# Kernel tuning notes

Measured on AMD Instinct MI355X. Metric: run time of the kernel, lower is better.

Reference implementation:

```python
import jax, jax.numpy as jnp
import numpy as np
from jax import lax

N, E, F, H, B = 16384, 262144, 32, 128, 16
DI, DS, DC, DTR = 256, 16, 4, 8   # Mamba: d_inner=expand*H, d_state, d_conv, dt_rank=ceil(H/16)
NS, NC = 512, 8                   # num_stations, num line colors
EPS = 1e-5


def _forward(node_features, edge_index, batch, W_in, b_in, W_g1, b_g1, W_g2, b_g2,
             W_inproj, conv_w, conv_b, W_xproj, W_dt, b_dt, A_log, D_p, W_out,
             gamma, beta, Wc, bc, Wh, bh, Wt, bt, Wp1, bp1, Wp2, bp2, Wd, bd, Ws, bs):
    def gcn(x, W, b):
        # GCNConv with self-loops and symmetric normalization
        loops = jnp.arange(N)
        s = jnp.concatenate([edge_index[0], loops])
        d = jnp.concatenate([edge_index[1], loops])
        deg = jax.ops.segment_sum(jnp.ones(s.shape[0], x.dtype), d, num_segments=N)
        dinv = jnp.where(deg > 0, lax.rsqrt(deg), 0.0)
        xw = x @ W
        msg = xw[s] * (dinv[s] * dinv[d])[:, None]
        return jax.ops.segment_sum(msg, d, num_segments=N) + b

    h = jax.nn.relu(node_features @ W_in + b_in)
    h = jax.nn.relu(gcn(h, W_g1, b_g1))
    h_gnn = jax.nn.relu(gcn(h, W_g2, b_g2))

    # --- Mamba block over the node sequence (batch dim of 1, seq_len = N) ---
    xz = h_gnn @ W_inproj                      # (N, 2*DI)
    x, z = xz[:, :DI], xz[:, DI:]
    xp = jnp.pad(x, ((DC - 1, 0), (0, 0)))     # causal depthwise conv1d
    xc = conv_b + sum(xp[k:k + N] * conv_w[:, k] for k in range(DC))
    x = jax.nn.silu(xc)
    dbl = x @ W_xproj                          # (N, DTR + 2*DS)
    dt = jax.nn.softplus(dbl[:, :DTR] @ W_dt + b_dt)   # (N, DI)
    Bm = dbl[:, DTR:DTR + DS]                  # (N, DS)
    Cm = dbl[:, DTR + DS:]                     # (N, DS)
    A = -jnp.exp(A_log)                        # (DI, DS)
    dA = jnp.exp(dt[:, :, None] * A[None])     # (N, DI, DS)
    dBx = dt[:, :, None] * Bm[:, None, :] * x[:, :, None]

    def step(hst, t):
        dA_t, dBx_t, C_t = t
        hst = dA_t * hst + dBx_t               # (DI, DS)
        return hst, hst @ C_t                  # (DI,)

    _, ys = lax.scan(step, jnp.zeros((DI, DS), x.dtype), (dA, dBx, Cm))
    y = (ys + D_p * x) * jax.nn.silu(z)
    h_mamba = y @ W_out                        # (N, H)

    # residual + LayerNorm
    hh = h_gnn + h_mamba
    mu = hh.mean(-1, keepdims=True)
    var = ((hh - mu) ** 2).mean(-1, keepdims=True)
    h_final = (hh - mu) * lax.rsqrt(var + EPS) * gamma + beta

    # global_mean_pool per graph
    counts = jax.ops.segment_sum(jnp.ones(N, h_final.dtype), batch, num_segments=B)
    ge = jax.ops.segment_sum(h_final, batch, num_segments=B) / jnp.maximum(counts, 1.0)[:, None]

    # critic + all policy heads, concatenated: [1,4,3,NS,NS,NS,NC]
    return jnp.concatenate([ge @ Wc + bc, ge @ Wh + bh, ge @ Wt + bt,
                            ge @ Wp1 + bp1, ge @ Wp2 + bp2, ge @ Wd + bd,
                            ge @ Ws + bs], axis=-1)


def setup_inputs() -> dict:
    key = jax.random.key(0)
    ks = list(jax.random.split(key, 20))
    p = lambda i, shape, s=0.02: jax.random.normal(ks[i], shape, jnp.float32) * s
    return dict(
        node_features=jax.random.normal(ks[0], (N, F), jnp.float32),
        edge_index=jax.random.randint(ks[1], (2, E), 0, N),
        batch=jnp.sort(jax.random.randint(ks[2], (N,), 0, B)),
        W_in=p(3, (F, H)), b_in=jnp.zeros((H,), jnp.float32),
        W_g1=p(4, (H, H)), b_g1=jnp.zeros((H,), jnp.float32),
        W_g2=p(5, (H, H)), b_g2=jnp.zeros((H,), jnp.float32),
        W_inproj=p(6, (H, 2 * DI)),
        conv_w=p(7, (DI, DC)), conv_b=jnp.zeros((DI,), jnp.float32),
        W_xproj=p(8, (DI, DTR + 2 * DS)),
        W_dt=p(9, (DTR, DI)), b_dt=jnp.full((DI,), -4.0, jnp.float32),
        A_log=jnp.log(jnp.broadcast_to(jnp.arange(1.0, DS + 1.0, dtype=jnp.float32), (DI, DS))),
        D_p=jnp.ones((DI,), jnp.float32),
        W_out=p(10, (DI, H)),
        gamma=jnp.ones((H,), jnp.float32), beta=jnp.zeros((H,), jnp.float32),
        Wc=p(11, (H, 1)), bc=jnp.zeros((1,), jnp.float32),
        Wh=p(12, (H, 4)), bh=jnp.zeros((4,), jnp.float32),
        Wt=p(13, (H, 3)), bt=jnp.zeros((3,), jnp.float32),
        Wp1=p(14, (H, NS)), bp1=jnp.zeros((NS,), jnp.float32),
        Wp2=p(15, (H, NS)), bp2=jnp.zeros((NS,), jnp.float32),
        Wd=p(16, (H, NS)), bd=jnp.zeros((NS,), jnp.float32),
        Ws=p(17, (H, NC)), bs=jnp.zeros((NC,), jnp.float32),
    )


def reference(node_features, edge_index, batch, W_in, b_in, W_g1, b_g1, W_g2, b_g2,
              W_inproj, conv_w, conv_b, W_xproj, W_dt, b_dt, A_log, D_p, W_out,
              gamma, beta, Wc, bc, Wh, bh, Wt, bt, Wp1, bp1, Wp2, bp2, Wd, bd, Ws, bs):
    return _forward(node_features, edge_index, batch, W_in, b_in, W_g1, b_g1, W_g2, b_g2,
                    W_inproj, conv_w, conv_b, W_xproj, W_dt, b_dt, A_log, D_p, W_out,
                    gamma, beta, Wc, bc, Wh, bh, Wt, bt, Wp1, bp1, Wp2, bp2, Wd, bd, Ws, bs)
```

## Files before the change

kernel.cpp:

```cpp
#include <hip/hip_runtime.h>
#include <math.h>

#define NN 16384
#define EE 262144
#define FF 32
#define HH 128
#define BB 16
#define DI 256
#define DS 16
#define DC 4
#define DTR 8
#define OUTW 1552
#define NCH 512
#define CHLEN 32

__device__ __forceinline__ float siluf(float v) { return v / (1.f + __expf(-v)); }
__device__ __forceinline__ float softplusf(float v) {
    return fmaxf(v, 0.f) + __logf(1.f + __expf(-fabsf(v)));
}

__global__ void zero_kernel(int* __restrict__ cnt, float* __restrict__ ge,
                            int* __restrict__ counts) {
    int idx = blockIdx.x * blockDim.x + threadIdx.x;
    if (idx < NN) cnt[idx] = 0;
    if (idx < BB * HH) ge[idx] = 0.f;
    if (idx < BB) counts[idx] = 0;
}

__global__ void deg_kernel(const int* __restrict__ dst, int* __restrict__ cnt) {
    int e = blockIdx.x * blockDim.x + threadIdx.x;
    if (e < EE) atomicAdd(&cnt[dst[e]], 1);
}

__global__ __launch_bounds__(1024) void prefix_kernel(const int* __restrict__ cnt,
                                                      int* __restrict__ rowptr,
                                                      int* __restrict__ cursor,
                                                      float* __restrict__ dinv) {
    __shared__ int part[1024];
    int tid = threadIdx.x;
    int4 c4[4];
#pragma unroll
    for (int j = 0; j < 4; j++) c4[j] = ((const int4*)cnt)[tid * 4 + j];
    int v[16] = {c4[0].x, c4[0].y, c4[0].z, c4[0].w, c4[1].x, c4[1].y, c4[1].z, c4[1].w,
                 c4[2].x, c4[2].y, c4[2].z, c4[2].w, c4[3].x, c4[3].y, c4[3].z, c4[3].w};
    int s = 0;
#pragma unroll
    for (int j = 0; j < 16; j++) s += v[j];
    part[tid] = s;
    __syncthreads();
    for (int off = 1; off < 1024; off <<= 1) {
        int t = (tid >= off) ? part[tid - off] : 0;
        __syncthreads();
        part[tid] += t;
        __syncthreads();
    }
    int running = part[tid] - s;
    int rp[16];
    float dv[16];
#pragma unroll
    for (int j = 0; j < 16; j++) {
        rp[j] = running;
        running += v[j];
        dv[j] = rsqrtf((float)(v[j] + 1));
    }
#pragma unroll
    for (int j = 0; j < 4; j++) {
        int4 r4; r4.x = rp[j*4]; r4.y = rp[j*4+1]; r4.z = rp[j*4+2]; r4.w = rp[j*4+3];
        ((int4*)rowptr)[tid * 4 + j] = r4;
        ((int4*)cursor)[tid * 4 + j] = r4;
        float4 d4; d4.x = dv[j*4]; d4.y = dv[j*4+1]; d4.z = dv[j*4+2]; d4.w = dv[j*4+3];
        ((float4*)dinv)[tid * 4 + j] = d4;
    }
    if (tid == 1023) rowptr[NN] = part[1023];
}

__global__ void scatter_kernel(const int* __restrict__ src, const int* __restrict__ dst,
                               int* __restrict__ cursor, int* __restrict__ col) {
    int e = blockIdx.x * blockDim.x + threadIdx.x;
    if (e < EE) {
        int d = dst[e];
        int pos = atomicAdd(&cursor[d], 1);
        col[pos] = src[e];
    }
}

__global__ __launch_bounds__(256) void gemm_k(const float* __restrict__ A,
                                              const float* __restrict__ B,
                                              const float* __restrict__ bias,
                                              float* __restrict__ C,
                                              int M, int Nn, int K, int act) {
    __shared__ float As[16][68];
    __shared__ float Bs[16][68];
    int tid = threadIdx.x;
    int m0 = blockIdx.y * 64;
    int n0 = blockIdx.x * 64;
    int ty = tid >> 4, tx = tid & 15;
    float acc[4][4] = {{0.f}};
    for (int k0 = 0; k0 < K; k0 += 16) {
#pragma unroll
        for (int l = 0; l < 4; l++) {
            int idx = tid + l * 256;
            int i = idx >> 4, j = idx & 15;
            As[j][i] = A[(size_t)(m0 + i) * K + k0 + j];
        }
#pragma unroll
        for (int l = 0; l < 4; l++) {
            int idx = tid + l * 256;
            int i = idx >> 6, j = idx & 63;
            int n = n0 + j;
            Bs[i][j] = (n < Nn) ? B[(size_t)(k0 + i) * Nn + n] : 0.f;
        }
        __syncthreads();
#pragma unroll
        for (int kk = 0; kk < 16; kk++) {
            float4 a4 = *(const float4*)&As[kk][ty * 4];
            float4 b4 = *(const float4*)&Bs[kk][tx * 4];
            float av[4] = {a4.x, a4.y, a4.z, a4.w};
            float bv[4] = {b4.x, b4.y, b4.z, b4.w};
#pragma unroll
            for (int r = 0; r < 4; r++)
#pragma unroll
                for (int c = 0; c < 4; c++) acc[r][c] = fmaf(av[r], bv[c], acc[r][c]);
        }
        __syncthreads();
    }
    int nb = n0 + tx * 4;
    if (nb < Nn) {
        float4 bi4 = {0.f, 0.f, 0.f, 0.f};
        if (bias) bi4 = *(const float4*)&bias[nb];
#pragma unroll
        for (int r = 0; r < 4; r++) {
            int m = m0 + ty * 4 + r;
            float4 v;
            v.x = acc[r][0] + bi4.x; v.y = acc[r][1] + bi4.y;
            v.z = acc[r][2] + bi4.z; v.w = acc[r][3] + bi4.w;
            if (act == 1) {
                v.x = fmaxf(v.x, 0.f); v.y = fmaxf(v.y, 0.f);
                v.z = fmaxf(v.z, 0.f); v.w = fmaxf(v.w, 0.f);
            }
            *(float4*)&C[(size_t)m * Nn + nb] = v;
        }
    }
}

union SMemIn {
    struct { float Ns[64][33]; float Ws[32][132]; } s1;
    float Bs[16][68];
};

__global__ __launch_bounds__(256) void gemm_in_g1(const float* __restrict__ nf,
                                                  const float* __restrict__ W_in,
                                                  const float* __restrict__ b_in,
                                                  const float* __restrict__ W_g1,
                                                  float* __restrict__ out) {
    __shared__ SMemIn sm;
    __shared__ float Hs[128][68];
    int tid = threadIdx.x;
    int m0 = blockIdx.y * 64;
    int n0 = blockIdx.x * 64;
    int ty = tid >> 4, tx = tid & 15;
#pragma unroll
    for (int l = 0; l < 2; l++) {
        int q = tid + l * 256;
        int r = q >> 3, c4 = (q & 7) * 4;
        *(float4*)&sm.s1.Ns[r][c4] = *(const float4*)&nf[(size_t)(m0 + r) * FF + c4];
    }
#pragma unroll
    for (int l = 0; l < 4; l++) {
        int q = tid + l * 256;
        int r = q >> 5, c4 = (q & 31) * 4;
        *(float4*)&sm.s1.Ws[r][c4] = *(const float4*)&W_in[(size_t)r * HH + c4];
    }
    __syncthreads();
    {
        float4 b0 = *(const float4*)&b_in[tx * 4];
        float4 b1 = *(const float4*)&b_in[64 + tx * 4];
        float hacc[4][8];
#pragma unroll
        for (int r = 0; r < 4; r++) {
            hacc[r][0] = b0.x; hacc[r][1] = b0.y; hacc[r][2] = b0.z; hacc[r][3] = b0.w;
            hacc[r][4] = b1.x; hacc[r][5] = b1.y; hacc[r][6] = b1.z; hacc[r][7] = b1.w;
        }
#pragma unroll
        for (int k = 0; k < FF; k++) {
            float av[4];
#pragma unroll
            for (int r = 0; r < 4; r++) av[r] = sm.s1.Ns[ty * 4 + r][k];
            float wv[8];
#pragma unroll
            for (int c = 0; c < 4; c++) {
                wv[c]     = sm.s1.Ws[k][tx * 4 + c];
                wv[c + 4] = sm.s1.Ws[k][64 + tx * 4 + c];
            }
#pragma unroll
            for (int r = 0; r < 4; r++)
#pragma unroll
                for (int c = 0; c < 8; c++) hacc[r][c] = fmaf(av[r], wv[c], hacc[r][c]);
        }
#pragma unroll
        for (int r = 0; r < 4; r++)
#pragma unroll
            for (int c = 0; c < 4; c++) {
                Hs[tx * 4 + c][ty * 4 + r]      = fmaxf(hacc[r][c], 0.f);
                Hs[64 + tx * 4 + c][ty * 4 + r] = fmaxf(hacc[r][c + 4], 0.f);
            }
    }
    __syncthreads();
    float acc[4][4] = {{0.f}};
    for (int k0 = 0; k0 < HH; k0 += 16) {
        *(float4*)&sm.Bs[tid >> 4][(tid & 15) * 4] =
            *(const float4*)&W_g1[(size_t)(k0 + (tid >> 4)) * HH + n0 + (tid & 15) * 4];
        __syncthreads();
#pragma unroll
        for (int kk = 0; kk < 16; kk++) {
            float4 a4 = *(const float4*)&Hs[k0 + kk][ty * 4];
            float4 b4 = *(const float4*)&sm.Bs[kk][tx * 4];
            float av[4] = {a4.x, a4.y, a4.z, a4.w};
            float bv[4] = {b4.x, b4.y, b4.z, b4.w};
#pragma unroll
            for (int r = 0; r < 4; r++)
#pragma unroll
                for (int c = 0; c < 4; c++) acc[r][c] = fmaf(av[r], bv[c], acc[r][c]);
        }
        __syncthreads();
    }
#pragma unroll
    for (int r = 0; r < 4; r++) {
        int m = m0 + ty * 4 + r;
        float4 v;
        v.x = acc[r][0]; v.y = acc[r][1]; v.z = acc[r][2]; v.w = acc[r][3];
        *(float4*)&out[(size_t)m * HH + n0 + tx * 4] = v;
    }
}

__global__ __launch_bounds__(512, 4) void gemm_big512_t(const float* __restrict__ A,
                                                        const float* __restrict__ B,
                                                        float* __restrict__ CT,
                                                        int M, int Nn, int K) {
    __shared__ float As[16][132];
    __shared__ float Bs[16][132];
    int tid = threadIdx.x;
    int m0 = blockIdx.y * 128;
    int n0 = blockIdx.x * 128;
    int ty = tid >> 4;
    int tx = tid & 15;
    float acc[4][8] = {{0.f}};
    for (int k0 = 0; k0 < K; k0 += 16) {
        {
            int m = tid >> 2;
            int kc = (tid & 3) * 4;
            float4 a = *(const float4*)&A[(size_t)(m0 + m) * K + k0 + kc];
            As[kc + 0][m] = a.x; As[kc + 1][m] = a.y;
            As[kc + 2][m] = a.z; As[kc + 3][m] = a.w;
        }
        {
            int krow = tid >> 5;
            int c4 = (tid & 31) * 4;
            *(float4*)&Bs[krow][c4] = *(const float4*)&B[(size_t)(k0 + krow) * Nn + n0 + c4];
        }
        __syncthreads();
#pragma unroll
        for (int kk = 0; kk < 16; kk++) {
            float4 a4 = *(const float4*)&As[kk][ty * 4];
            float4 b0 = *(const float4*)&Bs[kk][tx * 4];
            float4 b1 = *(const float4*)&Bs[kk][64 + tx * 4];
            float av[4] = {a4.x, a4.y, a4.z, a4.w};
            float bv[8] = {b0.x, b0.y, b0.z, b0.w, b1.x, b1.y, b1.z, b1.w};
#pragma unroll
            for (int r = 0; r < 4; r++)
#pragma unroll
                for (int c = 0; c < 8; c++) acc[r][c] = fmaf(av[r], bv[c], acc[r][c]);
        }
        __syncthreads();
    }
#pragma unroll
    for (int cc = 0; cc < 4; cc++) {
        float4 v;
        v.x = acc[0][cc]; v.y = acc[1][cc]; v.z = acc[2][cc]; v.w = acc[3][cc];
        *(float4*)&CT[(size_t)(n0 + tx * 4 + cc) * NN + m0 + ty * 4] = v;
        float4 u;
        u.x = acc[0][cc + 4]; u.y = acc[1][cc + 4]; u.z = acc[2][cc + 4]; u.w = acc[3][cc + 4];
        *(float4*)&CT[(size_t)(n0 + 64 + tx * 4 + cc) * NN + m0 + ty * 4] = u;
    }
}

__global__ __launch_bounds__(256) void gemm_xz_dblt(const float* __restrict__ xzt,
                                                    const float* __restrict__ B,
                                                    const float* __restrict__ cw,
                                                    const float* __restrict__ cb,
                                                    float* __restrict__ xst,
                                                    float* __restrict__ dblt) {
    __shared__ float As[16][68];
    __shared__ float Bs[16][68];
    __shared__ float Raw[16][72];
    __shared__ float Ct[64][41];
    int tid = threadIdx.x;
    int m0 = blockIdx.x * 64;
    int ty = tid >> 4, tx = tid & 15;
    float acc[4][4] = {{0.f}};
    for (int k0 = 0; k0 < DI; k0 += 16) {
#pragma unroll
        for (int l = 0; l < 2; l++) {
            int idx = tid + l * 256;
            if (idx < 272) {
                int kk = idx / 17, j = idx % 17;
                int tcol = m0 - 4 + j * 4;
                float4 v;
                if (tcol >= 0) v = *(const float4*)&xzt[(size_t)(k0 + kk) * NN + tcol];
                else { v.x = 0.f; v.y = 0.f; v.z = 0.f; v.w = 0.f; }
                *(float4*)&Raw[kk][j * 4] = v;
            }
        }
#pragma unroll
        for (int l = 0; l < 4; l++) {
            int idx = tid + l * 256;
            int i2 = idx >> 6, j2 = idx & 63;
            Bs[i2][j2] = (j2 < 40) ? B[(size_t)(k0 + i2) * 40 + j2] : 0.f;
        }
        __syncthreads();
#pragma unroll
        for (int l = 0; l < 4; l++) {
            int kk = (tid >> 6) + l * 4;
            int i = tid & 63;
            int d = k0 + kk;
            float w0 = cw[d * DC + 0], w1 = cw[d * DC + 1];
            float w2 = cw[d * DC + 2], w3 = cw[d * DC + 3];
            float v = siluf(cb[d] + w0 * Raw[kk][i + 1] + w1 * Raw[kk][i + 2]
                                  + w2 * Raw[kk][i + 3] + w3 * Raw[kk][i + 4]);
            As[kk][i] = v;
            xst[(size_t)d * NN + m0 + i] = v;
        }
        __syncthreads();
#pragma unroll
        for (int kk = 0; kk < 16; kk++) {
            float4 a4 = *(const float4*)&As[kk][ty * 4];
            float4 b4 = *(const float4*)&Bs[kk][tx * 4];
            float av[4] = {a4.x, a4.y, a4.z, a4.w};
            float bv[4] = {b4.x, b4.y, b4.z, b4.w};
#pragma unroll
            for (int r = 0; r < 4; r++)
#pragma unroll
                for (int c = 0; c < 4; c++) acc[r][c] = fmaf(av[r], bv[c], acc[r][c]);
        }
        __syncthreads();
    }
    if (tx * 4 < 40) {
#pragma unroll
        for (int r = 0; r < 4; r++) {
            int m = ty * 4 + r;
            Ct[m][tx * 4 + 0] = acc[r][0];
            Ct[m][tx * 4 + 1] = acc[r][1];
            Ct[m][tx * 4 + 2] = acc[r][2];
            Ct[m][tx * 4 + 3] = acc[r][3];
        }
    }
    __syncthreads();
#pragma unroll
    for (int l = 0; l < 10; l++) {
        int idx = tid + l * 256;
        int n = idx >> 6, m = idx & 63;
        dblt[(size_t)n * NN + m0 + m] = Ct[m][n];
    }
}

__global__ __launch_bounds__(256) void gemm_at_ln_pool(const float* __restrict__ AT,
                                                       const float* __restrict__ B,
                                                       const float* __restrict__ hg,
                                                       const float* __restrict__ gamma,
                                                       const float* __restrict__ beta,
                                                       const int* __restrict__ batch,
                                                       float* __restrict__ ge,
                                                       int* __restrict__ counts) {
    __shared__ float As[16][36];
    __shared__ float Bs[16][132];
    __shared__ float lnb[32][132];
    __shared__ int gb[32];
    int tid = threadIdx.x;
    int m0 = blockIdx.x * 32;
    int ty = tid >> 4, tx = tid & 15;
    float acc[2][8] = {{0.f}};
    for (int k0 = 0; k0 < 256; k0 += 16) {
        {
            int idx = tid * 2;
            int kk = idx >> 5, i = idx & 31;
            As[kk][i] = AT[(size_t)(k0 + kk) * NN + m0 + i];
            As[kk][i + 1] = AT[(size_t)(k0 + kk) * NN + m0 + i + 1];
        }
        {
            int krow = tid >> 4;
            int c8 = (tid & 15) * 8;
            const float* bp = &B[(size_t)(k0 + krow) * HH + c8];
            *(float4*)&Bs[krow][c8] = *(const float4*)bp;
            *(float4*)&Bs[krow][c8 + 4] = *(const float4*)(bp + 4);
        }
        __syncthreads();
#pragma unroll
        for (int kk = 0; kk < 16; kk++) {
            float a0 = As[kk][ty * 2];
            float a1 = As[kk][ty * 2 + 1];
            float4 b0 = *(const float4*)&Bs[kk][tx * 4];
            float4 b1 = *(const float4*)&Bs[kk][64 + tx * 4];
            float bv[8] = {b0.x, b0.y, b0.z, b0.w, b1.x, b1.y, b1.z, b1.w};
#pragma unroll
            for (int c = 0; c < 8; c++) {
                acc[0][c] = fmaf(a0, bv[c], acc[0][c]);
                acc[1][c] = fmaf(a1, bv[c], acc[1][c]);
            }
        }
        __syncthreads();
    }
    if (tid < 32) gb[tid] = batch[m0 + tid];
    float4 g0 = *(const float4*)&gamma[tx * 4];
    float4 g1 = *(const float4*)&gamma[64 + tx * 4];
    float4 be0 = *(const float4*)&beta[tx * 4];
    float4 be1 = *(const float4*)&beta[64 + tx * 4];
    float gv[8] = {g0.x, g0.y, g0.z, g0.w, g1.x, g1.y, g1.z, g1.w};
    float bv[8] = {be0.x, be0.y, be0.z, be0.w, be1.x, be1.y, be1.z, be1.w};
#pragma unroll
    for (int r = 0; r < 2; r++) {
        int m = m0 + ty * 2 + r;
        float4 h0 = *(const float4*)&hg[(size_t)m * HH + tx * 4];
        float4 h1 = *(const float4*)&hg[(size_t)m * HH + 64 + tx * 4];
        float v[8] = {acc[r][0] + h0.x, acc[r][1] + h0.y, acc[r][2] + h0.z, acc[r][3] + h0.w,
                      acc[r][4] + h1.x, acc[r][5] + h1.y, acc[r][6] + h1.z, acc[r][7] + h1.w};
        float sum = 0.f;
#pragma unroll
        for (int c = 0; c < 8; c++) sum += v[c];
        sum += __shfl_xor(sum, 1); sum += __shfl_xor(sum, 2);
        sum += __shfl_xor(sum, 4); sum += __shfl_xor(sum, 8);
        float mu = sum * (1.f / 128.f);
        float vs = 0.f;
#pragma unroll
        for (int c = 0; c < 8; c++) { float dd = v[c] - mu; vs += dd * dd; }
        vs += __shfl_xor(vs, 1); vs += __shfl_xor(vs, 2);
        vs += __shfl_xor(vs, 4); vs += __shfl_xor(vs, 8);
        float inv = rsqrtf(vs * (1.f / 128.f) + 1e-5f);
        int lr = ty * 2 + r;
        float4 o0, o1;
        o0.x = (v[0] - mu) * inv * gv[0] + bv[0];
        o0.y = (v[1] - mu) * inv * gv[1] + bv[1];
        o0.z = (v[2] - mu) * inv * gv[2] + bv[2];
        o0.w = (v[3] - mu) * inv * gv[3] + bv[3];
        o1.x = (v[4] - mu) * inv * gv[4] + bv[4];
        o1.y = (v[5] - mu) * inv * gv[5] + bv[5];
        o1.z = (v[6] - mu) * inv * gv[6] + bv[6];
        o1.w = (v[7] - mu) * inv * gv[7] + bv[7];
        *(float4*)&lnb[lr][tx * 4] = o0;
        *(float4*)&lnb[lr][64 + tx * 4] = o1;
    }
    __syncthreads();
    if (tid < HH) {
        int f = tid;
        int gcur = gb[0];
        float acc2 = 0.f;
        int cnt = 0;
#pragma unroll 4
        for (int i = 0; i < 32; i++) {
            int g = gb[i];
            if (g != gcur) {
                atomicAdd(&ge[gcur * HH + f], acc2);
                if (f == 0) atomicAdd(&counts[gcur], cnt);
                acc2 = 0.f; cnt = 0; gcur = g;
            }
            acc2 += lnb[i][f];
            cnt++;
        }
        atomicAdd(&ge[gcur * HH + f], acc2);
        if (f == 0) atomicAdd(&counts[gcur], cnt);
    }
}

__global__ __launch_bounds__(256) void gcn_gather4(const float* __restrict__ xw,
                                                   const int* __restrict__ rowptr,
                                                   const int* __restrict__ col,
                                                   const float* __restrict__ dinv,
                                                   const float* __restrict__ b,
                                                   float* __restrict__ out) {
    int tid = threadIdx.x;
    int sub = tid & 31;
    int n = blockIdx.x * 8 + (tid >> 5);
    float dn = dinv[n];
    const float4* xw4 = (const float4*)xw;
    float4 a = xw4[(size_t)n * 32 + sub];
    float ws = dn * dn;
    float4 acc;
    acc.x = a.x * ws; acc.y = a.y * ws; acc.z = a.z * ws; acc.w = a.w * ws;
    int beg = rowptr[n], end = rowptr[n + 1];
    int e = beg;
    for (; e + 4 <= end; e += 4) {
        int s0 = col[e], s1 = col[e + 1], s2 = col[e + 2], s3 = col[e + 3];
        float w0 = dinv[s0] * dn, w1 = dinv[s1] * dn;
        float w2 = dinv[s2] * dn, w3 = dinv[s3] * dn;
        float4 v0 = xw4[(size_t)s0 * 32 + sub];
        float4 v1 = xw4[(size_t)s1 * 32 + sub];
        float4 v2 = xw4[(size_t)s2 * 32 + sub];
        float4 v3 = xw4[(size_t)s3 * 32 + sub];
        acc.x = fmaf(v0.x, w0, acc.x); acc.y = fmaf(v0.y, w0, acc.y);
        acc.z = fmaf(v0.z, w0, acc.z); acc.w = fmaf(v0.w, w0, acc.w);
        acc.x = fmaf(v1.x, w1, acc.x); acc.y = fmaf(v1.y, w1, acc.y);
        acc.z = fmaf(v1.z, w1, acc.z); acc.w = fmaf(v1.w, w1, acc.w);
        acc.x = fmaf(v2.x, w2, acc.x); acc.y = fmaf(v2.y, w2, acc.y);
        acc.z = fmaf(v2.z, w2, acc.z); acc.w = fmaf(v2.w, w2, acc.w);
        acc.x = fmaf(v3.x, w3, acc.x); acc.y = fmaf(v3.y, w3, acc.y);
        acc.z = fmaf(v3.z, w3, acc.z); acc.w = fmaf(v3.w, w3, acc.w);
    }
    for (; e < end; e++) {
        int s0 = col[e];
        float w0 = dinv[s0] * dn;
        float4 v0 = xw4[(size_t)s0 * 32 + sub];
        acc.x = fmaf(v0.x, w0, acc.x); acc.y = fmaf(v0.y, w0, acc.y);
        acc.z = fmaf(v0.z, w0, acc.z); acc.w = fmaf(v0.w, w0, acc.w);
    }
    float4 b4 = ((const float4*)b)[sub];
    acc.x = fmaxf(acc.x + b4.x, 0.f);
    acc.y = fmaxf(acc.y + b4.y, 0.f);
    acc.z = fmaxf(acc.z + b4.z, 0.f);
    acc.w = fmaxf(acc.w + b4.w, 0.f);
    ((float4*)out)[(size_t)n * 32 + sub] = acc;
}

__global__ __launch_bounds__(256) void scan_phase1(const float* __restrict__ xst,
                                                   const float* __restrict__ dblt,
                                                   const float* __restrict__ A_log,
                                                   const float* __restrict__ W_dt,
                                                   const float* __restrict__ b_dt,
                                                   float* __restrict__ chkP,
                                                   float* __restrict__ chkH) {
    __shared__ float Tx[CHLEN][257];
    __shared__ float D8s[8][33];
    __shared__ float Bt[CHLEN][20];
    int tid = threadIdx.x;
    int chunk = blockIdx.x;
    int t0 = chunk * CHLEN;
#pragma unroll
    for (int jj = 0; jj < 32; jj++) {
        int lin = tid + jj * 256;
        int dd = lin >> 5, t = lin & 31;
        Tx[t][dd] = xst[(size_t)dd * NN + t0 + t];
    }
    {
        int s = tid >> 5, t = tid & 31;
        D8s[s][t] = dblt[(size_t)s * NN + t0 + t];
    }
#pragma unroll
    for (int jj = 0; jj < 2; jj++) {
        int lin = tid + jj * 256;
        int s = lin >> 5, t = lin & 31;
        Bt[t][s] = dblt[(size_t)(8 + s) * NN + t0 + t];
    }
    int d = tid;
    float wv[8];
#pragma unroll
    for (int k = 0; k < 8; k++) wv[k] = W_dt[k * DI + d];
    float bd = b_dt[d];
    float A[16];
#pragma unroll
    for (int q = 0; q < 4; q++) {
        float4 al = *(const float4*)&A_log[d * DS + q * 4];
        A[q*4+0] = -expf(al.x); A[q*4+1] = -expf(al.y);
        A[q*4+2] = -expf(al.z); A[q*4+3] = -expf(al.w);
    }
    float h[16], P[16];
#pragma unroll
    for (int s = 0; s < 16; s++) { h[s] = 0.f; P[s] = 1.f; }
    __syncthreads();
    for (int t = 0; t < CHLEN; t++) {
        float acc = bd;
#pragma unroll
        for (int k = 0; k < 8; k++) acc = fmaf(D8s[k][t], wv[k], acc);
        float dtv = softplusf(acc);
        float dx = dtv * Tx[t][d];
        float4 b0 = *(const float4*)&Bt[t][0];
        float4 b1 = *(const float4*)&Bt[t][4];
        float4 b2 = *(const float4*)&Bt[t][8];
        float4 b3 = *(const float4*)&Bt[t][12];
        float Bv[16] = {b0.x,b0.y,b0.z,b0.w, b1.x,b1.y,b1.z,b1.w,
                        b2.x,b2.y,b2.z,b2.w, b3.x,b3.y,b3.z,b3.w};
#pragma unroll
        for (int s = 0; s < 16; s++) {
            float a = __expf(dtv * A[s]);
            h[s] = fmaf(a, h[s], dx * Bv[s]);
            P[s] *= a;
        }
    }
    size_t base = (size_t)chunk * 4096 + d * 16;
#pragma unroll
    for (int q = 0; q < 4; q++) {
        float4 vP; vP.x = P[q*4]; vP.y = P[q*4+1]; vP.z = P[q*4+2]; vP.w = P[q*4+3];
        float4 vH; vH.x = h[q*4]; vH.y = h[q*4+1]; vH.z = h[q*4+2]; vH.w = h[q*4+3];
        *(float4*)&chkP[base + q*4] = vP;
        *(float4*)&chkH[base + q*4] = vH;
    }
}

__global__ void scan_phase2(const float* chkP, const float* chkH, float* init) {
    int idx = blockIdx.x * blockDim.x + threadIdx.x;
    float h = 0.f;
    float p[8], q[8], pn[8], qn[8];
#pragma unroll
    for (int j = 0; j < 8; j++) {
        p[j] = chkP[j * 4096 + idx];
        q[j] = chkH[j * 4096 + idx];
    }
    for (int c0 = 0; c0 < NCH; c0 += 8) {
        if (c0 + 8 < NCH) {
#pragma unroll
            for (int j = 0; j < 8; j++) {
                pn[j] = chkP[(c0 + 8 + j) * 4096 + idx];
                qn[j] = chkH[(c0 + 8 + j) * 4096 + idx];
            }
        }
#pragma unroll
        for (int j = 0; j < 8; j++) {
            init[(c0 + j) * 4096 + idx] = h;
            h = fmaf(p[j], h, q[j]);
        }
#pragma unroll
        for (int j = 0; j < 8; j++) { p[j] = pn[j]; q[j] = qn[j]; }
    }
}

__global__ __launch_bounds__(256) void scan_phase3(const float* __restrict__ xst,
                                                   const float* __restrict__ dblt,
                                                   const float* __restrict__ A_log,
                                                   const float* __restrict__ W_dt,
                                                   const float* __restrict__ b_dt,
                                                   const float* __restrict__ init,
                                                   const float* __restrict__ D_p,
                                                   const float* __restrict__ xzt,
                                                   float* __restrict__ yt) {
    __shared__ float Tx[CHLEN][257];
    __shared__ float Yl[CHLEN][257];
    __shared__ float D8s[8][33];
    __shared__ float Bt[CHLEN][20];
    __shared__ float Ctt[CHLEN][20];
    int tid = threadIdx.x;
    int chunk = blockIdx.x;
    int t0 = chunk * CHLEN;
#pragma unroll
    for (int jj = 0; jj < 32; jj++) {
        int lin = tid + jj * 256;
        int dd = lin >> 5, t = lin & 31;
        Tx[t][dd] = xst[(size_t)dd * NN + t0 + t];
    }
    {
        int s = tid >> 5, t = tid & 31;
        D8s[s][t] = dblt[(size_t)s * NN + t0 + t];
    }
#pragma unroll
    for (int jj = 0; jj < 2; jj++) {
        int lin = tid + jj * 256;
        int s = lin >> 5, t = lin & 31;
        Bt[t][s]  = dblt[(size_t)(8 + s) * NN + t0 + t];
        Ctt[t][s] = dblt[(size_t)(24 + s) * NN + t0 + t];
    }
    int d = tid;
    float wv[8];
#pragma unroll
    for (int k = 0; k < 8; k++) wv[k] = W_dt[k * DI + d];
    float bd = b_dt[d];
    float Dd = D_p[d];
    float A[16];
#pragma unroll
    for (int q = 0; q < 4; q++) {
        float4 al = *(const float4*)&A_log[d * DS + q * 4];
        A[q*4+0] = -expf(al.x); A[q*4+1] = -expf(al.y);
        A[q*4+2] = -expf(al.z); A[q*4+3] = -expf(al.w);
    }
    float h[16];
    size_t base = (size_t)chunk * 4096 + d * 16;
#pragma unroll
    for (int q = 0; q < 4; q++) {
        float4 vi = *(const float4*)&init[base + q * 4];
        h[q*4+0] = vi.x; h[q*4+1] = vi.y; h[q*4+2] = vi.z; h[q*4+3] = vi.w;
    }
    __syncthreads();
    for (int t = 0; t < CHLEN; t++) {
        float acc = bd;
#pragma unroll
        for (int k = 0; k < 8; k++) acc = fmaf(D8s[k][t], wv[k], acc);
        float dtv = softplusf(acc);
        float x = Tx[t][d];
        float dx = dtv * x;
        float4 b0 = *(const float4*)&Bt[t][0];
        float4 b1 = *(const float4*)&Bt[t][4];
        float4 b2 = *(const float4*)&Bt[t][8];
        float4 b3 = *(const float4*)&Bt[t][12];
        float4 c0 = *(const float4*)&Ctt[t][0];
        float4 c1 = *(const float4*)&Ctt[t][4];
        float4 c2 = *(const float4*)&Ctt[t][8];
        float4 c3 = *(const float4*)&Ctt[t][12];
        float Bv[16] = {b0.x,b0.y,b0.z,b0.w, b1.x,b1.y,b1.z,b1.w,
                        b2.x,b2.y,b2.z,b2.w, b3.x,b3.y,b3.z,b3.w};
        float Cv[16] = {c0.x,c0.y,c0.z,c0.w, c1.x,c1.y,c1.z,c1.w,
                        c2.x,c2.y,c2.z,c2.w, c3.x,c3.y,c3.z,c3.w};
        float y = 0.f;
#pragma unroll
        for (int s = 0; s < 16; s++) {
            float a = __expf(dtv * A[s]);
            h[s] = fmaf(a, h[s], dx * Bv[s]);
            y = fmaf(h[s], Cv[s], y);
        }
        Yl[t][d] = fmaf(Dd, x, y);
    }
    __syncthreads();
#pragma unroll
    for (int jj = 0; jj < 32; jj++) {
        int lin = tid + jj * 256;
        int dd = lin >> 5, t = lin & 31;
        float z = xzt[(size_t)(256 + dd) * NN + t0 + t];
        yt[(size_t)dd * NN + t0 + t] = Yl[t][dd] * siluf(z);
    }
}

__global__ void heads_kernel(const float* __restrict__ ge, const int* __restrict__ counts,
                             const float* Wc, const float* bc, const float* Wh, const float* bh,
                             const float* Wt, const float* bt, const float* Wp1, const float* bp1,
                             const float* Wp2, const float* bp2, const float* Wd, const float* bd,
                             const float* Ws, const float* bs, float* __restrict__ out) {
    int col = blockIdx.x * blockDim.x + threadIdx.x;
    int b = blockIdx.y;
    if (col >= OUTW) return;
    const float* W; const float* bi; int lc, w;
    if (col < 1)         { W = Wc;  bi = bc;  lc = col;        w = 1; }
    else if (col < 5)    { W = Wh;  bi = bh;  lc = col - 1;    w = 4; }
    else if (col < 8)    { W = Wt;  bi = bt;  lc = col - 5;    w = 3; }
    else if (col < 520)  { W = Wp1; bi = bp1; lc = col - 8;    w = 512; }
    else if (col < 1032) { W = Wp2; bi = bp2; lc = col - 520;  w = 512; }
    else if (col < 1544) { W = Wd;  bi = bd;  lc = col - 1032; w = 512; }
    else                 { W = Ws;  bi = bs;  lc = col - 1544; w = 8; }
    float scale = 1.f / fmaxf((float)counts[b], 1.f);
    float dot = 0.f;
#pragma unroll 8
    for (int f = 0; f < HH; f++) dot = fmaf(ge[b * HH + f], W[f * w + lc], dot);
    out[(size_t)b * OUTW + col] = bi[lc] + scale * dot;
}

extern "C" void kernel_launch(void* const* d_in, const int* in_sizes, int n_in,
                              void* d_out, int out_size, void* d_ws, size_t ws_size,
                              hipStream_t stream) {
    const float* nf      = (const float*)d_in[0];
    const int*   ei      = (const int*)d_in[1];
    const int*   batch   = (const int*)d_in[2];
    const float* W_in    = (const float*)d_in[3];
    const float* b_in    = (const float*)d_in[4];
    const float* W_g1    = (const float*)d_in[5];
    const float* b_g1    = (const float*)d_in[6];
    const float* W_g2    = (const float*)d_in[7];
    const float* b_g2    = (const float*)d_in[8];
    const float* W_inproj= (const float*)d_in[9];
    const float* conv_w  = (const float*)d_in[10];
    const float* conv_b  = (const float*)d_in[11];
    const float* W_xproj = (const float*)d_in[12];
    const float* W_dt    = (const float*)d_in[13];
    const float* b_dt    = (const float*)d_in[14];
    const float* A_log   = (const float*)d_in[15];
    const float* D_p     = (const float*)d_in[16];
    const float* W_out   = (const float*)d_in[17];
    const float* gamma   = (const float*)d_in[18];
    const float* beta    = (const float*)d_in[19];
    const float* Wc = (const float*)d_in[20]; const float* bc = (const float*)d_in[21];
    const float* Wh = (const float*)d_in[22]; const float* bh = (const float*)d_in[23];
    const float* Wt = (const float*)d_in[24]; const float* bt = (const float*)d_in[25];
    const float* Wp1= (const float*)d_in[26]; const float* bp1= (const float*)d_in[27];
    const float* Wp2= (const float*)d_in[28]; const float* bp2= (const float*)d_in[29];
    const float* Wd = (const float*)d_in[30]; const float* bd = (const float*)d_in[31];
    const float* Ws = (const float*)d_in[32]; const float* bs = (const float*)d_in[33];

    const int* e_src = ei;
    const int* e_dst = ei + EE;

    float* w = (float*)d_ws;
    size_t o = 0;
    float* F0   = w + o; o += (size_t)NN * HH;
    float* F1   = w + o; o += (size_t)NN * HH;
    float* F2   = w + o; o += (size_t)NN * HH;
    float* XZT  = w + o; o += (size_t)NN * 512;
    float* YT   = XZT;
    float* XST  = w + o; o += (size_t)NN * DI;
    float* DBLT = w + o; o += (size_t)NN * 40;
    float* GE   = w + o; o += BB * HH;
    float* DINV = w + o; o += NN;
    int* ip = (int*)(w + o);
    int* CNT    = ip; ip += NN;
    int* ROWPTR = ip; ip += NN + 1;
    int* CURSOR = ip; ip += NN;
    int* COL    = ip; ip += EE;
    int* COUNTS = ip; ip += BB;

    float* CHP  = F0;
    float* CHH  = F1;
    float* INI  = CHP;

    zero_kernel<<<(NN + 255) / 256, 256, 0, stream>>>(CNT, GE, COUNTS);

    deg_kernel<<<EE / 256, 256, 0, stream>>>(e_dst, CNT);
    prefix_kernel<<<1, 1024, 0, stream>>>(CNT, ROWPTR, CURSOR, DINV);
    scatter_kernel<<<EE / 256, 256, 0, stream>>>(e_src, e_dst, CURSOR, COL);

    gemm_in_g1<<<dim3(2, NN / 64), 256, 0, stream>>>(nf, W_in, b_in, W_g1, F1);
    gcn_gather4<<<NN / 8, 256, 0, stream>>>(F1, ROWPTR, COL, DINV, b_g1, F0);
    gemm_k<<<dim3(2, NN / 64), 256, 0, stream>>>(F0, W_g2, nullptr, F1, NN, HH, HH, 0);
    gcn_gather4<<<NN / 8, 256, 0, stream>>>(F1, ROWPTR, COL, DINV, b_g2, F2);

    gemm_big512_t<<<dim3(4, NN / 128), 512, 0, stream>>>(F2, W_inproj, XZT, NN, 512, HH);
    gemm_xz_dblt<<<NN / 64, 256, 0, stream>>>(XZT, W_xproj, conv_w, conv_b, XST, DBLT);

    scan_phase1<<<NCH, 256, 0, stream>>>(XST, DBLT, A_log, W_dt, b_dt, CHP, CHH);
    scan_phase2<<<16, 256, 0, stream>>>(CHP, CHH, INI);
    scan_phase3<<<NCH, 256, 0, stream>>>(XST, DBLT, A_log, W_dt, b_dt, INI, D_p, XZT, YT);

    gemm_at_ln_pool<<<NN / 32, 256, 0, stream>>>(YT, W_out, F2, gamma, beta, batch, GE, COUNTS);

    heads_kernel<<<dim3((OUTW + 127) / 128, BB), 128, 0, stream>>>(
        GE, COUNTS, Wc, bc, Wh, bh, Wt, bt, Wp1, bp1, Wp2, bp2, Wd, bd, Ws, bs, (float*)d_out);
}
```

Before: 418.9 us.

## Split conv/silu into row kernel, vectorize scan loads, retile scan chunk state layout

```diff
diff --git a/kernel.cpp b/kernel.cpp
--- a/kernel.cpp
+++ b/kernel.cpp
@@ -284,15 +284,40 @@
     }
 }
 
-__global__ __launch_bounds__(256) void gemm_xz_dblt(const float* __restrict__ xzt,
+__global__ __launch_bounds__(256) void conv_silu_rows(const float* __restrict__ xzt,
+                                                      const float* __restrict__ cw,
+                                                      const float* __restrict__ cb,
+                                                      float* __restrict__ xst,
+                                                      float* __restrict__ szt) {
+    int d = blockIdx.y;
+    int tg = blockIdx.x * 1024 + threadIdx.x * 4;
+    const float* row = xzt + (size_t)d * NN;
+    float4 cur = *(const float4*)&row[tg];
+    if (d < DI) {
+        float4 prev;
+        if (tg == 0) { prev.x = 0.f; prev.y = 0.f; prev.z = 0.f; prev.w = 0.f; }
+        else prev = *(const float4*)&row[tg - 4];
+        float w0 = cw[d * DC + 0], w1 = cw[d * DC + 1];
+        float w2 = cw[d * DC + 2], w3 = cw[d * DC + 3];
+        float b = cb[d];
+        float4 o;
+        o.x = siluf(b + w0 * prev.y + w1 * prev.z + w2 * prev.w + w3 * cur.x);
+        o.y = siluf(b + w0 * prev.z + w1 * prev.w + w2 * cur.x + w3 * cur.y);
+        o.z = siluf(b + w0 * prev.w + w1 * cur.x + w2 * cur.y + w3 * cur.z);
+        o.w = siluf(b + w0 * cur.x + w1 * cur.y + w2 * cur.z + w3 * cur.w);
+        *(float4*)&xst[(size_t)d * NN + tg] = o;
+    } else {
+        float4 o;
+        o.x = siluf(cur.x); o.y = siluf(cur.y); o.z = siluf(cur.z); o.w = siluf(cur.w);
+        *(float4*)&szt[(size_t)(d - DI) * NN + tg] = o;
+    }
+}
+
+__global__ __launch_bounds__(256) void gemm_at_dblt(const float* __restrict__ AT,
                                                     const float* __restrict__ B,
-                                                    const float* __restrict__ cw,
-                                                    const float* __restrict__ cb,
-                                                    float* __restrict__ xst,
                                                     float* __restrict__ dblt) {
     __shared__ float As[16][68];
     __shared__ float Bs[16][68];
-    __shared__ float Raw[16][72];
     __shared__ float Ct[64][41];
     int tid = threadIdx.x;
     int m0 = blockIdx.x * 64;
@@ -300,35 +325,16 @@
     float acc[4][4] = {{0.f}};
     for (int k0 = 0; k0 < DI; k0 += 16) {
 #pragma unroll
-        for (int l = 0; l < 2; l++) {
-            int idx = tid + l * 256;
-            if (idx < 272) {
-                int kk = idx / 17, j = idx % 17;
-                int tcol = m0 - 4 + j * 4;
-                float4 v;
-                if (tcol >= 0) v = *(const float4*)&xzt[(size_t)(k0 + kk) * NN + tcol];
-                else { v.x = 0.f; v.y = 0.f; v.z = 0.f; v.w = 0.f; }
-                *(float4*)&Raw[kk][j * 4] = v;
-            }
-        }
-#pragma unroll
         for (int l = 0; l < 4; l++) {
             int idx = tid + l * 256;
-            int i2 = idx >> 6, j2 = idx & 63;
-            Bs[i2][j2] = (j2 < 40) ? B[(size_t)(k0 + i2) * 40 + j2] : 0.f;
-        }
-        __syncthreads();
+            int kk = idx >> 6, i = idx & 63;
+            As[kk][i] = AT[(size_t)(k0 + kk) * NN + m0 + i];
+        }
 #pragma unroll
         for (int l = 0; l < 4; l++) {
-            int kk = (tid >> 6) + l * 4;
-            int i = tid & 63;
-            int d = k0 + kk;
-            float w0 = cw[d * DC + 0], w1 = cw[d * DC + 1];
-            float w2 = cw[d * DC + 2], w3 = cw[d * DC + 3];
-            float v = siluf(cb[d] + w0 * Raw[kk][i + 1] + w1 * Raw[kk][i + 2]
-                                  + w2 * Raw[kk][i + 3] + w3 * Raw[kk][i + 4]);
-            As[kk][i] = v;
-            xst[(size_t)d * NN + m0 + i] = v;
+            int idx = tid + l * 256;
+            int i = idx >> 6, j = idx & 63;
+            Bs[i][j] = (j < 40) ? B[(size_t)(k0 + i) * 40 + j] : 0.f;
         }
         __syncthreads();
 #pragma unroll
@@ -533,20 +539,24 @@
     int chunk = blockIdx.x;
     int t0 = chunk * CHLEN;
 #pragma unroll
-    for (int jj = 0; jj < 32; jj++) {
+    for (int jj = 0; jj < 8; jj++) {
         int lin = tid + jj * 256;
-        int dd = lin >> 5, t = lin & 31;
-        Tx[t][dd] = xst[(size_t)dd * NN + t0 + t];
-    }
-    {
-        int s = tid >> 5, t = tid & 31;
-        D8s[s][t] = dblt[(size_t)s * NN + t0 + t];
-    }
-#pragma unroll
-    for (int jj = 0; jj < 2; jj++) {
-        int lin = tid + jj * 256;
-        int s = lin >> 5, t = lin & 31;
-        Bt[t][s] = dblt[(size_t)(8 + s) * NN + t0 + t];
+        int dd = lin >> 3, tq = (lin & 7) * 4;
+        float4 v = *(const float4*)&xst[(size_t)dd * NN + t0 + tq];
+        Tx[tq + 0][dd] = v.x; Tx[tq + 1][dd] = v.y;
+        Tx[tq + 2][dd] = v.z; Tx[tq + 3][dd] = v.w;
+    }
+    if (tid < 128) {
+        int s = tid >> 3, tq = (tid & 7) * 4;
+        float4 v = *(const float4*)&dblt[(size_t)(8 + s) * NN + t0 + tq];
+        Bt[tq + 0][s] = v.x; Bt[tq + 1][s] = v.y;
+        Bt[tq + 2][s] = v.z; Bt[tq + 3][s] = v.w;
+    } else if (tid < 192) {
+        int l = tid - 128;
+        int s = l >> 3, tq = (l & 7) * 4;
+        float4 v = *(const float4*)&dblt[(size_t)s * NN + t0 + tq];
+        D8s[s][tq + 0] = v.x; D8s[s][tq + 1] = v.y;
+        D8s[s][tq + 2] = v.z; D8s[s][tq + 3] = v.w;
     }
     int d = tid;
     float wv[8];
@@ -557,13 +567,14 @@
 #pragma unroll
     for (int q = 0; q < 4; q++) {
         float4 al = *(const float4*)&A_log[d * DS + q * 4];
-        A[q*4+0] = -expf(al.x); A[q*4+1] = -expf(al.y);
-        A[q*4+2] = -expf(al.z); A[q*4+3] = -expf(al.w);
+        A[q * 4 + 0] = -expf(al.x); A[q * 4 + 1] = -expf(al.y);
+        A[q * 4 + 2] = -expf(al.z); A[q * 4 + 3] = -expf(al.w);
     }
     float h[16], P[16];
 #pragma unroll
     for (int s = 0; s < 16; s++) { h[s] = 0.f; P[s] = 1.f; }
     __syncthreads();
+#pragma unroll 4
     for (int t = 0; t < CHLEN; t++) {
         float acc = bd;
 #pragma unroll
@@ -583,40 +594,54 @@
             P[s] *= a;
         }
     }
-    size_t base = (size_t)chunk * 4096 + d * 16;
-#pragma unroll
-    for (int q = 0; q < 4; q++) {
-        float4 vP; vP.x = P[q*4]; vP.y = P[q*4+1]; vP.z = P[q*4+2]; vP.w = P[q*4+3];
-        float4 vH; vH.x = h[q*4]; vH.y = h[q*4+1]; vH.z = h[q*4+2]; vH.w = h[q*4+3];
-        *(float4*)&chkP[base + q*4] = vP;
-        *(float4*)&chkH[base + q*4] = vH;
+    size_t base = (size_t)chunk * 4096 + d;
+#pragma unroll
+    for (int s = 0; s < 16; s++) {
+        chkP[base + s * 256] = P[s];
+        chkH[base + s * 256] = h[s];
     }
 }
 
 __global__ void scan_phase2(const float* chkP, const float* chkH, float* init) {
     int idx = blockIdx.x * blockDim.x + threadIdx.x;
     float h = 0.f;
-    float p[8], q[8], pn[8], qn[8];
+    float p0[8], q0[8], p1[8], q1[8], p2[8], q2[8], p3[8], q3[8];
 #pragma unroll
     for (int j = 0; j < 8; j++) {
-        p[j] = chkP[j * 4096 + idx];
-        q[j] = chkH[j * 4096 + idx];
-    }
-    for (int c0 = 0; c0 < NCH; c0 += 8) {
-        if (c0 + 8 < NCH) {
-#pragma unroll
-            for (int j = 0; j < 8; j++) {
-                pn[j] = chkP[(c0 + 8 + j) * 4096 + idx];
-                qn[j] = chkH[(c0 + 8 + j) * 4096 + idx];
-            }
-        }
-#pragma unroll
-        for (int j = 0; j < 8; j++) {
-            init[(c0 + j) * 4096 + idx] = h;
-            h = fmaf(p[j], h, q[j]);
-        }
-#pragma unroll
-        for (int j = 0; j < 8; j++) { p[j] = pn[j]; q[j] = qn[j]; }
+        p0[j] = chkP[(0 * 8 + j) * 4096 + idx]; q0[j] = chkH[(0 * 8 + j) * 4096 + idx];
+        p1[j] = chkP[(1 * 8 + j) * 4096 + idx]; q1[j] = chkH[(1 * 8 + j) * 4096 + idx];
+        p2[j] = chkP[(2 * 8 + j) * 4096 + idx]; q2[j] = chkH[(2 * 8 + j) * 4096 + idx];
+        p3[j] = chkP[(3 * 8 + j) * 4096 + idx]; q3[j] = chkH[(3 * 8 + j) * 4096 + idx];
+    }
+    for (int g = 0; g < 64; g += 4) {
+#pragma unroll
+        for (int j = 0; j < 8; j++) { init[((g + 0) * 8 + j) * 4096 + idx] = h; h = fmaf(p0[j], h, q0[j]); }
+        if (g + 4 < 64) {
+#pragma unroll
+            for (int j = 0; j < 8; j++) { p0[j] = chkP[((g + 4) * 8 + j) * 4096 + idx];
+                                          q0[j] = chkH[((g + 4) * 8 + j) * 4096 + idx]; }
+        }
+#pragma unroll
+        for (int j = 0; j < 8; j++) { init[((g + 1) * 8 + j) * 4096 + idx] = h; h = fmaf(p1[j], h, q1[j]); }
+        if (g + 5 < 64) {
+#pragma unroll
+            for (int j = 0; j < 8; j++) { p1[j] = chkP[((g + 5) * 8 + j) * 4096 + idx];
+                                          q1[j] = chkH[((g + 5) * 8 + j) * 4096 + idx]; }
+        }
+#pragma unroll
+        for (int j = 0; j < 8; j++) { init[((g + 2) * 8 + j) * 4096 + idx] = h; h = fmaf(p2[j], h, q2[j]); }
+        if (g + 6 < 64) {
+#pragma unroll
+            for (int j = 0; j < 8; j++) { p2[j] = chkP[((g + 6) * 8 + j) * 4096 + idx];
+                                          q2[j] = chkH[((g + 6) * 8 + j) * 4096 + idx]; }
+        }
+#pragma unroll
+        for (int j = 0; j < 8; j++) { init[((g + 3) * 8 + j) * 4096 + idx] = h; h = fmaf(p3[j], h, q3[j]); }
+        if (g + 7 < 64) {
+#pragma unroll
+            for (int j = 0; j < 8; j++) { p3[j] = chkP[((g + 7) * 8 + j) * 4096 + idx];
+                                          q3[j] = chkH[((g + 7) * 8 + j) * 4096 + idx]; }
+        }
     }
 }
 
@@ -627,10 +652,9 @@
                                                    const float* __restrict__ b_dt,
                                                    const float* __restrict__ init,
                                                    const float* __restrict__ D_p,
-                                                   const float* __restrict__ xzt,
+                                                   const float* __restrict__ szt,
                                                    float* __restrict__ yt) {
     __shared__ float Tx[CHLEN][257];
-    __shared__ float Yl[CHLEN][257];
     __shared__ float D8s[8][33];
     __shared__ float Bt[CHLEN][20];
     __shared__ float Ctt[CHLEN][20];
@@ -638,21 +662,30 @@
     int chunk = blockIdx.x;
     int t0 = chunk * CHLEN;
 #pragma unroll
-    for (int jj = 0; jj < 32; jj++) {
+    for (int jj = 0; jj < 8; jj++) {
         int lin = tid + jj * 256;
-        int dd = lin >> 5, t = lin & 31;
-        Tx[t][dd] = xst[(size_t)dd * NN + t0 + t];
-    }
-    {
-        int s = tid >> 5, t = tid & 31;
-        D8s[s][t] = dblt[(size_t)s * NN + t0 + t];
-    }
-#pragma unroll
-    for (int jj = 0; jj < 2; jj++) {
-        int lin = tid + jj * 256;
-        int s = lin >> 5, t = lin & 31;
-        Bt[t][s]  = dblt[(size_t)(8 + s) * NN + t0 + t];
-        Ctt[t][s] = dblt[(size_t)(24 + s) * NN + t0 + t];
+        int dd = lin >> 3, tq = (lin & 7) * 4;
+        float4 v = *(const float4*)&xst[(size_t)dd * NN + t0 + tq];
+        Tx[tq + 0][dd] = v.x; Tx[tq + 1][dd] = v.y;
+        Tx[tq + 2][dd] = v.z; Tx[tq + 3][dd] = v.w;
+    }
+    if (tid < 128) {
+        int s = tid >> 3, tq = (tid & 7) * 4;
+        float4 v = *(const float4*)&dblt[(size_t)(8 + s) * NN + t0 + tq];
+        Bt[tq + 0][s] = v.x; Bt[tq + 1][s] = v.y;
+        Bt[tq + 2][s] = v.z; Bt[tq + 3][s] = v.w;
+    } else {
+        int l = tid - 128;
+        int s = l >> 3, tq = (l & 7) * 4;
+        float4 v = *(const float4*)&dblt[(size_t)(24 + s) * NN + t0 + tq];
+        Ctt[tq + 0][s] = v.x; Ctt[tq + 1][s] = v.y;
+        Ctt[tq + 2][s] = v.z; Ctt[tq + 3][s] = v.w;
+    }
+    if (tid < 64) {
+        int s = tid >> 3, tq = (tid & 7) * 4;
+        float4 v = *(const float4*)&dblt[(size_t)s * NN + t0 + tq];
+        D8s[s][tq + 0] = v.x; D8s[s][tq + 1] = v.y;
+        D8s[s][tq + 2] = v.z; D8s[s][tq + 3] = v.w;
     }
     int d = tid;
     float wv[8];
@@ -664,17 +697,15 @@
 #pragma unroll
     for (int q = 0; q < 4; q++) {
         float4 al = *(const float4*)&A_log[d * DS + q * 4];
-        A[q*4+0] = -expf(al.x); A[q*4+1] = -expf(al.y);
-        A[q*4+2] = -expf(al.z); A[q*4+3] = -expf(al.w);
+        A[q * 4 + 0] = -expf(al.x); A[q * 4 + 1] = -expf(al.y);
+        A[q * 4 + 2] = -expf(al.z); A[q * 4 + 3] = -expf(al.w);
     }
     float h[16];
-    size_t base = (size_t)chunk * 4096 + d * 16;
-#pragma unroll
-    for (int q = 0; q < 4; q++) {
-        float4 vi = *(const float4*)&init[base + q * 4];
-        h[q*4+0] = vi.x; h[q*4+1] = vi.y; h[q*4+2] = vi.z; h[q*4+3] = vi.w;
-    }
+    size_t ibase = (size_t)chunk * 4096 + d;
+#pragma unroll
+    for (int s = 0; s < 16; s++) h[s] = init[ibase + s * 256];
     __syncthreads();
+#pragma unroll 4
     for (int t = 0; t < CHLEN; t++) {
         float acc = bd;
 #pragma unroll
@@ -701,15 +732,20 @@
             h[s] = fmaf(a, h[s], dx * Bv[s]);
             y = fmaf(h[s], Cv[s], y);
         }
-        Yl[t][d] = fmaf(Dd, x, y);
+        Tx[t][d] = fmaf(Dd, x, y);
     }
     __syncthreads();
 #pragma unroll
-    for (int jj = 0; jj < 32; jj++) {
+    for (int jj = 0; jj < 8; jj++) {
         int lin = tid + jj * 256;
-        int dd = lin >> 5, t = lin & 31;
-        float z = xzt[(size_t)(256 + dd) * NN + t0 + t];
-        yt[(size_t)dd * NN + t0 + t] = Yl[t][dd] * siluf(z);
+        int dd = lin >> 3, tq = (lin & 7) * 4;
+        float4 sz = *(const float4*)&szt[(size_t)dd * NN + t0 + tq];
+        float4 o;
+        o.x = Tx[tq + 0][dd] * sz.x;
+        o.y = Tx[tq + 1][dd] * sz.y;
+        o.z = Tx[tq + 2][dd] * sz.z;
+        o.w = Tx[tq + 3][dd] * sz.w;
+        *(float4*)&yt[(size_t)dd * NN + t0 + tq] = o;
     }
 }
 
@@ -778,6 +814,7 @@
     float* XZT  = w + o; o += (size_t)NN * 512;
     float* YT   = XZT;
     float* XST  = w + o; o += (size_t)NN * DI;
+    float* SZT  = w + o; o += (size_t)NN * DI;
     float* DBLT = w + o; o += (size_t)NN * 40;
     float* GE   = w + o; o += BB * HH;
     float* DINV = w + o; o += NN;
@@ -804,11 +841,12 @@
     gcn_gather4<<<NN / 8, 256, 0, stream>>>(F1, ROWPTR, COL, DINV, b_g2, F2);
 
     gemm_big512_t<<<dim3(4, NN / 128), 512, 0, stream>>>(F2, W_inproj, XZT, NN, 512, HH);
-    gemm_xz_dblt<<<NN / 64, 256, 0, stream>>>(XZT, W_xproj, conv_w, conv_b, XST, DBLT);
+    conv_silu_rows<<<dim3(NN / 1024, 512), 256, 0, stream>>>(XZT, conv_w, conv_b, XST, SZT);
+    gemm_at_dblt<<<NN / 64, 256, 0, stream>>>(XST, W_xproj, DBLT);
 
     scan_phase1<<<NCH, 256, 0, stream>>>(XST, DBLT, A_log, W_dt, b_dt, CHP, CHH);
     scan_phase2<<<16, 256, 0, stream>>>(CHP, CHH, INI);
-    scan_phase3<<<NCH, 256, 0, stream>>>(XST, DBLT, A_log, W_dt, b_dt, INI, D_p, XZT, YT);
+    scan_phase3<<<NCH, 256, 0, stream>>>(XST, DBLT, A_log, W_dt, b_dt, INI, D_p, SZT, YT);
 
     gemm_at_ln_pool<<<NN / 32, 256, 0, stream>>>(YT, W_out, F2, gamma, beta, batch, GE, COUNTS);
 
```

Result: faster. 398.2 us (-4.9%).
